# Kernel tuning notes

Measured on AMD Instinct MI355X. Metric: run time of the kernel, lower is better.

## Reference

```python
import jax, jax.numpy as jnp
import numpy as np

N, E = 50000, 800000
IN_DIM, HID, L, H = 128, 128, 3, 4
C = HID // H  # per-head channels
NEG_SLOPE = 0.2


def layer_norm(x, g, b, eps=1e-5):
    mu = jnp.mean(x, axis=-1, keepdims=True)
    var = jnp.var(x, axis=-1, keepdims=True)
    return (x - mu) * jax.lax.rsqrt(var + eps) * g + b


def gatv2_conv(x, edge_index, Wl, bl, Wr, br, att, conv_b):
    # x: [N, HID]; edge_index: [2, E]; Wl/Wr: [HID, HID]; att: [H, C]
    src, dst = edge_index[0], edge_index[1]
    xl = (x @ Wl + bl).reshape(N, H, C)  # source transform
    xr = (x @ Wr + br).reshape(N, H, C)  # target transform
    e = jax.nn.leaky_relu(xl[src] + xr[dst], NEG_SLOPE)      # [E, H, C]
    alpha = jnp.einsum('ehc,hc->eh', e, att)                  # [E, H]
    # segment softmax over incoming edges of each dst node
    amax = jax.ops.segment_max(alpha, dst, num_segments=N)    # [N, H]
    ex = jnp.exp(alpha - amax[dst])
    denom = jax.ops.segment_sum(ex, dst, num_segments=N)[dst] + 1e-16
    w = ex / denom                                            # [E, H]
    out = jax.ops.segment_sum(xl[src] * w[:, :, None], dst, num_segments=N)
    return out.reshape(N, HID) + conv_b


def setup_inputs() -> dict:
    key = jax.random.key(0)
    ks = jax.random.split(key, 24)
    s = 0.05
    inp = {
        'x': jax.random.normal(ks[0], (N, IN_DIM), jnp.float32),
        'edge_index': jax.random.randint(ks[1], (2, E), 0, N, jnp.int64),
        'Win': jax.random.normal(ks[2], (IN_DIM, HID)) * s,
        'b_in': jnp.zeros((HID,)),
        'ln_g': jnp.ones((L, HID)),
        'ln_b': jnp.zeros((L, HID)),
        'Wl': jax.random.normal(ks[3], (L, HID, HID)) * s,
        'bl': jnp.zeros((L, HID)),
        'Wr': jax.random.normal(ks[4], (L, HID, HID)) * s,
        'br': jnp.zeros((L, HID)),
        'att': jax.random.normal(ks[5], (L, H, C)) * s,
        'conv_b': jnp.zeros((L, HID)),
        'fn_g': jnp.ones((HID,)),
        'fn_b': jnp.zeros((HID,)),
        'pW1': jax.random.normal(ks[6], (HID, HID // 2)) * s,
        'pb1': jnp.zeros((HID // 2,)),
        'pW2': jax.random.normal(ks[7], (HID // 2, 1)) * s,
        'pb2': jnp.zeros((1,)),
        'vW1': jax.random.normal(ks[8], (HID, HID // 2)) * s,
        'vb1': jnp.zeros((HID // 2,)),
        'vW2': jax.random.normal(ks[9], (HID // 2, HID)) * s,
        'vb2': jnp.zeros((HID,)),
    }
    return inp


def reference(x, edge_index, Win, b_in, ln_g, ln_b, Wl, bl, Wr, br, att, conv_b,
              fn_g, fn_b, pW1, pb1, pW2, pb2, vW1, vb1, vW2, vb2):
    h = x @ Win + b_in  # input_proj
    # GNNResidualBlock (assumed pre-norm residual): h = h + gelu(conv(LN(h)))
    for i in range(L):
        z = layer_norm(h, ln_g[i], ln_b[i])
        z = gatv2_conv(z, edge_index, Wl[i], bl[i], Wr[i], br[i], att[i], conv_b[i])
        h = h + jax.nn.gelu(z)
    h = layer_norm(h, fn_g, fn_b)
    prob_logits = jax.nn.gelu(h @ pW1 + pb1) @ pW2 + pb2   # [N, 1]
    volume_emb = jax.nn.gelu(h @ vW1 + vb1) @ vW2 + vb2     # [N, HID]
    return (volume_emb, prob_logits)
```

## Files before the change

kernel.cpp:

```cpp
#include <hip/hip_runtime.h>
#include <math.h>

constexpr int NN  = 50000;
constexpr int EE  = 800000;

typedef short bf16x8 __attribute__((ext_vector_type(8)));
typedef float f32x4  __attribute__((ext_vector_type(4)));

__device__ __forceinline__ unsigned f2bfu(float f) {
    union { float f; unsigned u; } x; x.f = f;
    unsigned r = x.u + 0x7fffu + ((x.u >> 16) & 1u);
    return r >> 16;
}
__device__ __forceinline__ short f2bf(float f) { return (short)f2bfu(f); }
__device__ __forceinline__ unsigned pack2(float lo, float hi) {
    return f2bfu(lo) | (f2bfu(hi) << 16);
}
__device__ __forceinline__ float bfbits_lo(unsigned w) { return __uint_as_float(w << 16); }
__device__ __forceinline__ float bfbits_hi(unsigned w) { return __uint_as_float(w & 0xffff0000u); }

__device__ __forceinline__ float gelu_tanh(float x) {
    float u = 0.7978845608028654f * (x + 0.044715f * x * x * x);
    float t = 1.0f - 2.0f / (__expf(2.0f * u) + 1.0f);
    return 0.5f * x * (1.0f + t);
}

__device__ __forceinline__ float dpp_add16(float x) {
    int t;
    t = __builtin_amdgcn_update_dpp(0, __float_as_int(x), 0xB1,  0xf, 0xf, true);
    x += __int_as_float(t);
    t = __builtin_amdgcn_update_dpp(0, __float_as_int(x), 0x4E,  0xf, 0xf, true);
    x += __int_as_float(t);
    t = __builtin_amdgcn_update_dpp(0, __float_as_int(x), 0x141, 0xf, 0xf, true);
    x += __int_as_float(t);
    t = __builtin_amdgcn_update_dpp(0, __float_as_int(x), 0x140, 0xf, 0xf, true);
    x += __int_as_float(t);
    return x;
}

struct WtArgs {
    const float* src[10];
    short*       dst[10];
    int K[10];
    int N[10];
};

__global__ __launch_bounds__(256) void prep_weights(WtArgs a) {
    int m = blockIdx.x >> 4;
    int slice = blockIdx.x & 15;
    const float* s = a.src[m];
    short* d = a.dst[m];
    int K = a.K[m], N = a.N[m], total = K * N;
    for (int i = slice * 256 + threadIdx.x; i < total; i += 16 * 256) {
        int k = i / N, n = i - k * N;
        d[n * K + k] = f2bf(s[i]);
    }
}

template<int BN, int NB, int DO_LN, int ACT, int OUTBF0, int OUTBF1>
__global__ __launch_bounds__(256) void fused_ln_gemm(
    const float* __restrict__ A,
    const float* __restrict__ lg, const float* __restrict__ lb,
    const short* __restrict__ B0t, const float* __restrict__ bias0, void* __restrict__ C0,
    const short* __restrict__ B1t, const float* __restrict__ bias1, void* __restrict__ C1,
    int nrows)
{
    constexpr int K = 128, KP = 136, BM = 64;
    constexpr int NF = BN / 16;
    constexpr int CH = K / 8;
    __shared__ short As[BM * KP];
    __shared__ short Bs[BN * KP];

    const int tid  = threadIdx.x;
    const int row0 = blockIdx.x * BM;

    {
        int r = tid >> 2, q = tid & 3;
        int grow = row0 + r;
        bool ok = grow < nrows;
        float4 v[8];
        const float* src = A + (size_t)grow * K + q * 32;
#pragma unroll
        for (int i = 0; i < 8; ++i)
            v[i] = ok ? *reinterpret_cast<const float4*>(src + i * 4)
                      : make_float4(0.f, 0.f, 0.f, 0.f);
        if (DO_LN) {
            float s = 0.f, s2 = 0.f;
#pragma unroll
            for (int i = 0; i < 8; ++i) {
                s  += v[i].x + v[i].y + v[i].z + v[i].w;
                s2 += v[i].x * v[i].x + v[i].y * v[i].y + v[i].z * v[i].z + v[i].w * v[i].w;
            }
            s += __shfl_xor(s, 1); s2 += __shfl_xor(s2, 1);
            s += __shfl_xor(s, 2); s2 += __shfl_xor(s2, 2);
            float mean = s * (1.f / 128.f);
            float var  = s2 * (1.f / 128.f) - mean * mean;
            float rstd = rsqrtf(var + 1e-5f);
#pragma unroll
            for (int i = 0; i < 8; ++i) {
                float4 gg = *reinterpret_cast<const float4*>(lg + q * 32 + i * 4);
                float4 bb = *reinterpret_cast<const float4*>(lb + q * 32 + i * 4);
                v[i].x = (v[i].x - mean) * rstd * gg.x + bb.x;
                v[i].y = (v[i].y - mean) * rstd * gg.y + bb.y;
                v[i].z = (v[i].z - mean) * rstd * gg.z + bb.z;
                v[i].w = (v[i].w - mean) * rstd * gg.w + bb.w;
            }
        }
        short* dst = &As[r * KP + q * 32];
#pragma unroll
        for (int i = 0; i < 4; ++i) {
            uint4 w = make_uint4(pack2(v[2*i].x,   v[2*i].y),
                                 pack2(v[2*i].z,   v[2*i].w),
                                 pack2(v[2*i+1].x, v[2*i+1].y),
                                 pack2(v[2*i+1].z, v[2*i+1].w));
            *reinterpret_cast<uint4*>(dst + i * 8) = w;
        }
    }

    auto stageB = [&](const short* __restrict__ Bt) {
#pragma unroll
        for (int it = 0; it < BN * CH / 256; ++it) {
            int idx = tid + it * 256;
            int nn = idx / CH, j = idx % CH;
            *reinterpret_cast<uint4*>(&Bs[nn * KP + j * 8]) =
                *reinterpret_cast<const uint4*>(&Bt[nn * K + j * 8]);
        }
    };
    stageB(B0t);
    __syncthreads();

    const int wave = tid >> 6;
    const int lane = tid & 63;
    const int kg   = lane >> 4;
    const int lr   = lane & 15;

    bf16x8 afrag[4];
#pragma unroll
    for (int kk = 0; kk < 4; ++kk)
        afrag[kk] = *reinterpret_cast<const bf16x8*>(
            &As[(wave * 16 + lr) * KP + kk * 32 + kg * 8]);

    auto do_gemm = [&](const float* __restrict__ bias, void* __restrict__ Cv, bool outbf) {
        f32x4 acc[NF];
#pragma unroll
        for (int nf = 0; nf < NF; ++nf) acc[nf] = (f32x4){0.f, 0.f, 0.f, 0.f};
#pragma unroll
        for (int nf = 0; nf < NF; ++nf) {
#pragma unroll
            for (int kk = 0; kk < 4; ++kk) {
                bf16x8 bfrag = *reinterpret_cast<const bf16x8*>(
                    &Bs[(nf * 16 + lr) * KP + kk * 32 + kg * 8]);
                acc[nf] = __builtin_amdgcn_mfma_f32_16x16x32_bf16(
                    afrag[kk], bfrag, acc[nf], 0, 0, 0);
            }
        }
#pragma unroll
        for (int nf = 0; nf < NF; ++nf) {
            int col = nf * 16 + lr;
            float bi = bias[col];
#pragma unroll
            for (int j = 0; j < 4; ++j) {
                int row = row0 + wave * 16 + kg * 4 + j;
                if (row < nrows) {
                    float v = acc[nf][j] + bi;
                    if (ACT == 1) v = gelu_tanh(v);
                    if (outbf) ((short*)Cv)[(size_t)row * BN + col] = f2bf(v);
                    else       ((float*)Cv)[(size_t)row * BN + col] = v;
                }
            }
        }
    };

    do_gemm(bias0, C0, OUTBF0 != 0);
    if (NB == 2) {
        __syncthreads();
        stageB(B1t);
        __syncthreads();
        do_gemm(bias1, C1, OUTBF1 != 0);
    }
}

__global__ __launch_bounds__(256) void final_head_kernel(
    const float* __restrict__ A,
    const float* __restrict__ lg, const float* __restrict__ lb,
    const short* __restrict__ pW1t, const float* __restrict__ pb1,
    const float* __restrict__ pW2, const float* __restrict__ pb2,
    const short* __restrict__ vW1t, const float* __restrict__ vb1,
    short* __restrict__ t2, float* __restrict__ prob, int nrows)
{
    constexpr int K = 128, KP = 136, BM = 64;
    constexpr int CH = K / 8;
    __shared__ short As[BM * KP];
    __shared__ short Bs[128 * KP];

    const int tid  = threadIdx.x;
    const int row0 = blockIdx.x * BM;

    {
        int r = tid >> 2, q = tid & 3;
        int grow = row0 + r;
        bool ok = grow < nrows;
        float4 v[8];
        const float* src = A + (size_t)grow * K + q * 32;
#pragma unroll
        for (int i = 0; i < 8; ++i)
            v[i] = ok ? *reinterpret_cast<const float4*>(src + i * 4)
                      : make_float4(0.f, 0.f, 0.f, 0.f);
        float s = 0.f, s2 = 0.f;
#pragma unroll
        for (int i = 0; i < 8; ++i) {
            s  += v[i].x + v[i].y + v[i].z + v[i].w;
            s2 += v[i].x * v[i].x + v[i].y * v[i].y + v[i].z * v[i].z + v[i].w * v[i].w;
        }
        s += __shfl_xor(s, 1); s2 += __shfl_xor(s2, 1);
        s += __shfl_xor(s, 2); s2 += __shfl_xor(s2, 2);
        float mean = s * (1.f / 128.f);
        float var  = s2 * (1.f / 128.f) - mean * mean;
        float rstd = rsqrtf(var + 1e-5f);
        short* dst = &As[r * KP + q * 32];
#pragma unroll
        for (int i = 0; i < 8; ++i) {
            float4 gg = *reinterpret_cast<const float4*>(lg + q * 32 + i * 4);
            float4 bb = *reinterpret_cast<const float4*>(lb + q * 32 + i * 4);
            v[i].x = (v[i].x - mean) * rstd * gg.x + bb.x;
            v[i].y = (v[i].y - mean) * rstd * gg.y + bb.y;
            v[i].z = (v[i].z - mean) * rstd * gg.z + bb.z;
            v[i].w = (v[i].w - mean) * rstd * gg.w + bb.w;
        }
#pragma unroll
        for (int i = 0; i < 4; ++i) {
            uint4 w = make_uint4(pack2(v[2*i].x,   v[2*i].y),
                                 pack2(v[2*i].z,   v[2*i].w),
                                 pack2(v[2*i+1].x, v[2*i+1].y),
                                 pack2(v[2*i+1].z, v[2*i+1].w));
            *reinterpret_cast<uint4*>(dst + i * 8) = w;
        }
    }
#pragma unroll
    for (int it = 0; it < 8; ++it) {
        int idx = tid + it * 256;
        int nn = idx / CH, j = idx % CH;
        const short* srcw = (nn < 64) ? &pW1t[nn * K + j * 8]
                                      : &vW1t[(nn - 64) * K + j * 8];
        *reinterpret_cast<uint4*>(&Bs[nn * KP + j * 8]) =
            *reinterpret_cast<const uint4*>(srcw);
    }
    __syncthreads();

    const int wave = tid >> 6;
    const int lane = tid & 63;
    const int kg   = lane >> 4;
    const int lr   = lane & 15;

    bf16x8 afrag[4];
#pragma unroll
    for (int kk = 0; kk < 4; ++kk)
        afrag[kk] = *reinterpret_cast<const bf16x8*>(
            &As[(wave * 16 + lr) * KP + kk * 32 + kg * 8]);

    {
        f32x4 acc[4];
#pragma unroll
        for (int nf = 0; nf < 4; ++nf) acc[nf] = (f32x4){0.f, 0.f, 0.f, 0.f};
#pragma unroll
        for (int nf = 0; nf < 4; ++nf)
#pragma unroll
            for (int kk = 0; kk < 4; ++kk) {
                bf16x8 bfrag = *reinterpret_cast<const bf16x8*>(
                    &Bs[(64 + nf * 16 + lr) * KP + kk * 32 + kg * 8]);
                acc[nf] = __builtin_amdgcn_mfma_f32_16x16x32_bf16(
                    afrag[kk], bfrag, acc[nf], 0, 0, 0);
            }
#pragma unroll
        for (int nf = 0; nf < 4; ++nf) {
            int col = nf * 16 + lr;
            float bi = vb1[col];
#pragma unroll
            for (int j = 0; j < 4; ++j) {
                int row = row0 + wave * 16 + kg * 4 + j;
                if (row < nrows)
                    t2[(size_t)row * 64 + col] = f2bf(gelu_tanh(acc[nf][j] + bi));
            }
        }
    }
    {
        f32x4 acc[4];
#pragma unroll
        for (int nf = 0; nf < 4; ++nf) acc[nf] = (f32x4){0.f, 0.f, 0.f, 0.f};
#pragma unroll
        for (int nf = 0; nf < 4; ++nf)
#pragma unroll
            for (int kk = 0; kk < 4; ++kk) {
                bf16x8 bfrag = *reinterpret_cast<const bf16x8*>(
                    &Bs[(nf * 16 + lr) * KP + kk * 32 + kg * 8]);
                acc[nf] = __builtin_amdgcn_mfma_f32_16x16x32_bf16(
                    afrag[kk], bfrag, acc[nf], 0, 0, 0);
            }
        float pr[4] = {0.f, 0.f, 0.f, 0.f};
#pragma unroll
        for (int nf = 0; nf < 4; ++nf) {
            int col = nf * 16 + lr;
            float bi = pb1[col];
            float w2 = pW2[col];
#pragma unroll
            for (int j = 0; j < 4; ++j)
                pr[j] = fmaf(gelu_tanh(acc[nf][j] + bi), w2, pr[j]);
        }
#pragma unroll
        for (int j = 0; j < 4; ++j) {
            float v = dpp_add16(pr[j]);
            int row = row0 + wave * 16 + kg * 4 + j;
            if (lr == 0 && row < nrows) prob[row] = v + pb2[0];
        }
    }
}

template<int K, int BN, int ACT, int OUTBF>
__global__ __launch_bounds__(256) void gemm_mfma(
    const short* __restrict__ A, const short* __restrict__ Wt,
    const float* __restrict__ bias, void* __restrict__ Cv, int nrows)
{
    constexpr int BM = 64;
    constexpr int KP = K + 8;
    constexpr int NF = BN / 16;
    constexpr int KK = K / 32;
    constexpr int CH = K / 8;
    __shared__ short As[BM * KP];
    __shared__ short Bs[BN * KP];

    const int tid  = threadIdx.x;
    const int row0 = blockIdx.x * BM;

#pragma unroll
    for (int it = 0; it < BM * CH / 256; ++it) {
        int idx = tid + it * 256;
        int r = idx / CH, j = idx % CH;
        uint4 v = make_uint4(0u, 0u, 0u, 0u);
        if (row0 + r < nrows)
            v = *reinterpret_cast<const uint4*>(&A[(size_t)(row0 + r) * K + j * 8]);
        *reinterpret_cast<uint4*>(&As[r * KP + j * 8]) = v;
    }
#pragma unroll
    for (int it = 0; it < BN * CH / 256; ++it) {
        int idx = tid + it * 256;
        int n = idx / CH, j = idx % CH;
        *reinterpret_cast<uint4*>(&Bs[n * KP + j * 8]) =
            *reinterpret_cast<const uint4*>(&Wt[n * K + j * 8]);
    }
    __syncthreads();

    const int wave = tid >> 6;
    const int lane = tid & 63;
    const int kg   = lane >> 4;
    const int lr   = lane & 15;

    f32x4 acc[NF];
#pragma unroll
    for (int nf = 0; nf < NF; ++nf) acc[nf] = (f32x4){0.f, 0.f, 0.f, 0.f};

    bf16x8 afrag[KK];
#pragma unroll
    for (int kk = 0; kk < KK; ++kk)
        afrag[kk] = *reinterpret_cast<const bf16x8*>(
            &As[(wave * 16 + lr) * KP + kk * 32 + kg * 8]);

#pragma unroll
    for (int nf = 0; nf < NF; ++nf) {
#pragma unroll
        for (int kk = 0; kk < KK; ++kk) {
            bf16x8 bfrag = *reinterpret_cast<const bf16x8*>(
                &Bs[(nf * 16 + lr) * KP + kk * 32 + kg * 8]);
            acc[nf] = __builtin_amdgcn_mfma_f32_16x16x32_bf16(
                afrag[kk], bfrag, acc[nf], 0, 0, 0);
        }
    }

#pragma unroll
    for (int nf = 0; nf < NF; ++nf) {
        int col = nf * 16 + lr;
        float bi = bias[col];
#pragma unroll
        for (int j = 0; j < 4; ++j) {
            int row = row0 + wave * 16 + kg * 4 + j;
            if (row < nrows) {
                float v = acc[nf][j] + bi;
                if (ACT == 1) v = gelu_tanh(v);
                if (OUTBF) ((short*)Cv)[(size_t)row * BN + col] = f2bf(v);
                else       ((float*)Cv)[(size_t)row * BN + col] = v;
            }
        }
    }
}

__global__ void pos_kernel(const int* __restrict__ ei, int* __restrict__ counts,
                           int* __restrict__ pos) {
    int e = blockIdx.x * 256 + threadIdx.x;
    if (e < EE) pos[e] = atomicAdd(&counts[ei[EE + e]], 1);
}

__global__ __launch_bounds__(1024) void scan_kernel(const int* __restrict__ counts,
                                                    int* __restrict__ roff) {
    __shared__ int wsum[16];
    __shared__ int tilesum;
    int tid = threadIdx.x, wid = tid >> 6, lane = tid & 63;
    if (tid == 0) roff[0] = 0;
    int carry = 0;
    for (int base = 0; base < NN; base += 1024) {
        int idx = base + tid;
        int x = (idx < NN) ? counts[idx] : 0;
#pragma unroll
        for (int off = 1; off < 64; off <<= 1) {
            int t = __shfl_up(x, off);
            if (lane >= off) x += t;
        }
        if (lane == 63) wsum[wid] = x;
        __syncthreads();
        if (wid == 0) {
            int s = (lane < 16) ? wsum[lane] : 0;
#pragma unroll
            for (int off = 1; off < 16; off <<= 1) {
                int t = __shfl_up(s, off);
                if (lane >= off) s += t;
            }
            if (lane < 16) wsum[lane] = s;
            if (lane == 15) tilesum = s;
        }
        __syncthreads();
        int excl = (wid > 0) ? wsum[wid - 1] : 0;
        if (idx < NN) roff[idx + 1] = carry + excl + x;
        carry += tilesum;
        __syncthreads();
    }
}

__global__ void scatter_kernel(const int* __restrict__ ei, const int* __restrict__ roff,
                               const int* __restrict__ pos, int* __restrict__ ssrc) {
    int e = blockIdx.x * 256 + threadIdx.x;
    if (e < EE) {
        int d = ei[EE + e];
        ssrc[roff[d] + pos[e]] = ei[e] << 8;
    }
}

__global__ __launch_bounds__(256) void gat_node_kernel(
    const short* __restrict__ XL, const short* __restrict__ XR,
    const int* __restrict__ roff, const int* __restrict__ ssrc,
    const float* __restrict__ att, const float* __restrict__ conv_b,
    float* __restrict__ h)
{
    int n = blockIdx.x * 4 + (threadIdx.x >> 6);
    if (n >= NN) return;
    int lane = threadIdx.x & 63;
    int j0 = lane * 2;
    unsigned wr = *reinterpret_cast<const unsigned*>(&XR[(size_t)n * 128 + j0]);
    float xr0 = bfbits_lo(wr), xr1 = bfbits_hi(wr);
    float2 at = *reinterpret_cast<const float2*>(&att[j0]);

    float dA = 0.f, a0A = 0.f, a1A = 0.f;
    float dB = 0.f, a0B = 0.f, a1B = 0.f;

    const char* XLb = (const char*)XL;
    const unsigned lbyte = (unsigned)lane * 4u;

    auto proc = [&](unsigned w, float& d, float& a0, float& a1) {
        float x0 = bfbits_lo(w), x1 = bfbits_hi(w);
        float e0 = x0 + xr0; e0 = fmaxf(e0, 0.2f * e0);
        float e1 = x1 + xr1; e1 = fmaxf(e1, 0.2f * e1);
        float part = fmaf(e1, at.y, e0 * at.x);
        part = dpp_add16(part);
        float pe = __expf(part);
        d += pe;
        a0 = fmaf(pe, x0, a0);
        a1 = fmaf(pe, x1, a1);
    };

    int beg = roff[n], end = roff[n + 1], p = beg;
    for (; p + 3 < end; p += 4) {
        unsigned o0 = (unsigned)ssrc[p]     + lbyte;
        unsigned o1 = (unsigned)ssrc[p + 1] + lbyte;
        unsigned o2 = (unsigned)ssrc[p + 2] + lbyte;
        unsigned o3 = (unsigned)ssrc[p + 3] + lbyte;
        unsigned w0 = *reinterpret_cast<const unsigned*>(XLb + o0);
        unsigned w1 = *reinterpret_cast<const unsigned*>(XLb + o1);
        unsigned w2 = *reinterpret_cast<const unsigned*>(XLb + o2);
        unsigned w3 = *reinterpret_cast<const unsigned*>(XLb + o3);
        proc(w0, dA, a0A, a1A);
        proc(w1, dB, a0B, a1B);
        proc(w2, dA, a0A, a1A);
        proc(w3, dB, a0B, a1B);
    }
    for (; p < end; ++p) {
        unsigned w0 = *reinterpret_cast<const unsigned*>(
            XLb + ((unsigned)ssrc[p] + lbyte));
        proc(w0, dA, a0A, a1A);
    }
    float d    = dA + dB;
    float acc0 = a0A + a0B;
    float acc1 = a1A + a1B;

    float inv = 1.f / (d + 1e-16f);
    float2 cb = *reinterpret_cast<const float2*>(&conv_b[j0]);
    float o0 = gelu_tanh(fmaf(acc0, inv, cb.x));
    float o1 = gelu_tanh(fmaf(acc1, inv, cb.y));
    float2 hv = *reinterpret_cast<const float2*>(&h[(size_t)n * 128 + j0]);
    hv.x += o0; hv.y += o1;
    *reinterpret_cast<float2*>(&h[(size_t)n * 128 + j0]) = hv;
}

extern "C" void kernel_launch(void* const* d_in, const int* in_sizes, int n_in,
                              void* d_out, int out_size, void* d_ws, size_t ws_size,
                              hipStream_t stream)
{
    const float* x      = (const float*)d_in[0];
    const int*   ei     = (const int*)  d_in[1];
    const float* Win    = (const float*)d_in[2];
    const float* b_in   = (const float*)d_in[3];
    const float* ln_g   = (const float*)d_in[4];
    const float* ln_b   = (const float*)d_in[5];
    const float* Wl     = (const float*)d_in[6];
    const float* bl     = (const float*)d_in[7];
    const float* Wr     = (const float*)d_in[8];
    const float* br     = (const float*)d_in[9];
    const float* att    = (const float*)d_in[10];
    const float* conv_b = (const float*)d_in[11];
    const float* fn_g   = (const float*)d_in[12];
    const float* fn_b   = (const float*)d_in[13];
    const float* pW1    = (const float*)d_in[14];
    const float* pb1    = (const float*)d_in[15];
    const float* pW2    = (const float*)d_in[16];
    const float* pb2    = (const float*)d_in[17];
    const float* vW1    = (const float*)d_in[18];
    const float* vb1    = (const float*)d_in[19];
    const float* vW2    = (const float*)d_in[20];
    const float* vb2    = (const float*)d_in[21];

    char* wp = (char*)d_ws;
    float* h   = (float*)wp;  wp += (size_t)NN * 128 * 4;
    short* XL  = (short*)wp;  wp += (size_t)NN * 128 * 2;
    short* XR  = (short*)wp;  wp += (size_t)NN * 128 * 2;
    int* counts = (int*)wp;   wp += (size_t)NN * 4;
    int* roff   = (int*)wp;   wp += (size_t)(NN + 16) * 4;
    int* pos    = (int*)wp;   wp += (size_t)EE * 4;
    int* ssrc   = (int*)wp;   wp += (size_t)EE * 4;
    short* Win_t = (short*)wp;
    short* Wl_t  = Win_t + 16384;
    short* Wr_t  = Wl_t + 3 * 16384;
    short* pW1_t = Wr_t + 3 * 16384;
    short* vW1_t = pW1_t + 8192;
    short* vW2_t = vW1_t + 8192;
    short* t2 = XL;
    float* vol  = (float*)d_out;
    float* prob = (float*)d_out + (size_t)NN * 128;

    WtArgs wa;
    wa.src[0] = Win;  wa.dst[0] = Win_t; wa.K[0] = 128; wa.N[0] = 128;
    for (int i = 0; i < 3; ++i) {
        wa.src[1 + i] = Wl + (size_t)i * 16384; wa.dst[1 + i] = Wl_t + i * 16384;
        wa.K[1 + i] = 128; wa.N[1 + i] = 128;
        wa.src[4 + i] = Wr + (size_t)i * 16384; wa.dst[4 + i] = Wr_t + i * 16384;
        wa.K[4 + i] = 128; wa.N[4 + i] = 128;
    }
    wa.src[7] = pW1; wa.dst[7] = pW1_t; wa.K[7] = 128; wa.N[7] = 64;
    wa.src[8] = vW1; wa.dst[8] = vW1_t; wa.K[8] = 128; wa.N[8] = 64;
    wa.src[9] = vW2; wa.dst[9] = vW2_t; wa.K[9] = 64;  wa.N[9] = 128;
    prep_weights<<<160, 256, 0, stream>>>(wa);

    hipMemsetAsync(counts, 0, (size_t)NN * sizeof(int), stream);
    pos_kernel<<<(EE + 255) / 256, 256, 0, stream>>>(ei, counts, pos);
    scan_kernel<<<1, 1024, 0, stream>>>(counts, roff);
    scatter_kernel<<<(EE + 255) / 256, 256, 0, stream>>>(ei, roff, pos, ssrc);

    const int gemm_grid = (NN + 63) / 64;
    const int row_grid  = (NN + 3) / 4;

    fused_ln_gemm<128, 1, 0, 0, 0, 0><<<gemm_grid, 256, 0, stream>>>(
        x, nullptr, nullptr, Win_t, b_in, h, nullptr, nullptr, nullptr, NN);

    for (int i = 0; i < 3; ++i) {
        fused_ln_gemm<128, 2, 1, 0, 1, 1><<<gemm_grid, 256, 0, stream>>>(
            h, ln_g + i * 128, ln_b + i * 128,
            Wl_t + i * 16384, bl + i * 128, XL,
            Wr_t + i * 16384, br + i * 128, XR, NN);
        gat_node_kernel<<<row_grid, 256, 0, stream>>>(
            XL, XR, roff, ssrc, att + i * 128, conv_b + i * 128, h);
    }

    final_head_kernel<<<gemm_grid, 256, 0, stream>>>(
        h, fn_g, fn_b, pW1_t, pb1, pW2, pb2, vW1_t, vb1, t2, prob, NN);

    gemm_mfma<64, 128, 0, 0><<<gemm_grid, 256, 0, stream>>>(t2, vW2_t, vb2, vol, NN);
}
```

Baseline: 414.9 us.

## Process four edges per wavefront with 16-byte row loads in GAT aggregation

Restructures the per-node GATv2 aggregation so each wavefront splits into four 16-lane groups. Each group handles a different incoming edge, and each lane loads 8 bf16 channels with a single 16-byte load instead of 2 channels per lane. The 32-channel head reduction becomes a 4-lane DPP reduction, and partial sums are combined across groups with shuffles before only 16 lanes write the output. This is meant to cut per-edge instruction and reduction overhead and use wider memory transactions, at the cost of idle lanes on tail iterations and extra cross-group shuffles.

```diff
diff --git a/kernel.cpp b/kernel.cpp
--- a/kernel.cpp
+++ b/kernel.cpp
@@ -34,6 +34,15 @@
     t = __builtin_amdgcn_update_dpp(0, __float_as_int(x), 0x141, 0xf, 0xf, true);
     x += __int_as_float(t);
     t = __builtin_amdgcn_update_dpp(0, __float_as_int(x), 0x140, 0xf, 0xf, true);
+    x += __int_as_float(t);
+    return x;
+}
+
+__device__ __forceinline__ float dpp_add4(float x) {
+    int t;
+    t = __builtin_amdgcn_update_dpp(0, __float_as_int(x), 0xB1, 0xf, 0xf, true);
+    x += __int_as_float(t);
+    t = __builtin_amdgcn_update_dpp(0, __float_as_int(x), 0x4E, 0xf, 0xf, true);
     x += __int_as_float(t);
     return x;
 }
@@ -450,61 +459,85 @@
 {
     int n = blockIdx.x * 4 + (threadIdx.x >> 6);
     if (n >= NN) return;
-    int lane = threadIdx.x & 63;
-    int j0 = lane * 2;
-    unsigned wr = *reinterpret_cast<const unsigned*>(&XR[(size_t)n * 128 + j0]);
-    float xr0 = bfbits_lo(wr), xr1 = bfbits_hi(wr);
-    float2 at = *reinterpret_cast<const float2*>(&att[j0]);
-
-    float dA = 0.f, a0A = 0.f, a1A = 0.f;
-    float dB = 0.f, a0B = 0.f, a1B = 0.f;
+    const int lane = threadIdx.x & 63;
+    const int slot = lane >> 4;
+    const int pos  = lane & 15;
+    const unsigned cboff = (unsigned)pos * 16u;
+
+    float xr[8];
+    {
+        uint4 w4 = *reinterpret_cast<const uint4*>(&XR[(size_t)n * 128 + pos * 8]);
+        xr[0] = bfbits_lo(w4.x); xr[1] = bfbits_hi(w4.x);
+        xr[2] = bfbits_lo(w4.y); xr[3] = bfbits_hi(w4.y);
+        xr[4] = bfbits_lo(w4.z); xr[5] = bfbits_hi(w4.z);
+        xr[6] = bfbits_lo(w4.w); xr[7] = bfbits_hi(w4.w);
+    }
+    float at[8];
+    {
+        float4 a0 = *reinterpret_cast<const float4*>(&att[pos * 8]);
+        float4 a1 = *reinterpret_cast<const float4*>(&att[pos * 8 + 4]);
+        at[0] = a0.x; at[1] = a0.y; at[2] = a0.z; at[3] = a0.w;
+        at[4] = a1.x; at[5] = a1.y; at[6] = a1.z; at[7] = a1.w;
+    }
+
+    float d = 0.f;
+    float acc[8];
+#pragma unroll
+    for (int c = 0; c < 8; ++c) acc[c] = 0.f;
 
     const char* XLb = (const char*)XL;
-    const unsigned lbyte = (unsigned)lane * 4u;
-
-    auto proc = [&](unsigned w, float& d, float& a0, float& a1) {
-        float x0 = bfbits_lo(w), x1 = bfbits_hi(w);
-        float e0 = x0 + xr0; e0 = fmaxf(e0, 0.2f * e0);
-        float e1 = x1 + xr1; e1 = fmaxf(e1, 0.2f * e1);
-        float part = fmaf(e1, at.y, e0 * at.x);
-        part = dpp_add16(part);
-        float pe = __expf(part);
+    const int beg = roff[n], end = roff[n + 1];
+
+    for (int p0 = beg; p0 < end; p0 += 4) {
+        int p = p0 + slot;
+        bool valid = p < end;
+        int pc = valid ? p : beg;
+        unsigned off = (unsigned)ssrc[pc] + cboff;
+        uint4 w4 = *reinterpret_cast<const uint4*>(XLb + off);
+        float xl[8];
+        xl[0] = bfbits_lo(w4.x); xl[1] = bfbits_hi(w4.x);
+        xl[2] = bfbits_lo(w4.y); xl[3] = bfbits_hi(w4.y);
+        xl[4] = bfbits_lo(w4.z); xl[5] = bfbits_hi(w4.z);
+        xl[6] = bfbits_lo(w4.w); xl[7] = bfbits_hi(w4.w);
+        float part = 0.f;
+#pragma unroll
+        for (int c = 0; c < 8; ++c) {
+            float e = xl[c] + xr[c];
+            e = fmaxf(e, 0.2f * e);
+            part = fmaf(e, at[c], part);
+        }
+        part = dpp_add4(part);
+        float pe = valid ? __expf(part) : 0.f;
         d += pe;
-        a0 = fmaf(pe, x0, a0);
-        a1 = fmaf(pe, x1, a1);
-    };
-
-    int beg = roff[n], end = roff[n + 1], p = beg;
-    for (; p + 3 < end; p += 4) {
-        unsigned o0 = (unsigned)ssrc[p]     + lbyte;
-        unsigned o1 = (unsigned)ssrc[p + 1] + lbyte;
-        unsigned o2 = (unsigned)ssrc[p + 2] + lbyte;
-        unsigned o3 = (unsigned)ssrc[p + 3] + lbyte;
-        unsigned w0 = *reinterpret_cast<const unsigned*>(XLb + o0);
-        unsigned w1 = *reinterpret_cast<const unsigned*>(XLb + o1);
-        unsigned w2 = *reinterpret_cast<const unsigned*>(XLb + o2);
-        unsigned w3 = *reinterpret_cast<const unsigned*>(XLb + o3);
-        proc(w0, dA, a0A, a1A);
-        proc(w1, dB, a0B, a1B);
-        proc(w2, dA, a0A, a1A);
-        proc(w3, dB, a0B, a1B);
-    }
-    for (; p < end; ++p) {
-        unsigned w0 = *reinterpret_cast<const unsigned*>(
-            XLb + ((unsigned)ssrc[p] + lbyte));
-        proc(w0, dA, a0A, a1A);
-    }
-    float d    = dA + dB;
-    float acc0 = a0A + a0B;
-    float acc1 = a1A + a1B;
-
-    float inv = 1.f / (d + 1e-16f);
-    float2 cb = *reinterpret_cast<const float2*>(&conv_b[j0]);
-    float o0 = gelu_tanh(fmaf(acc0, inv, cb.x));
-    float o1 = gelu_tanh(fmaf(acc1, inv, cb.y));
-    float2 hv = *reinterpret_cast<const float2*>(&h[(size_t)n * 128 + j0]);
-    hv.x += o0; hv.y += o1;
-    *reinterpret_cast<float2*>(&h[(size_t)n * 128 + j0]) = hv;
+#pragma unroll
+        for (int c = 0; c < 8; ++c) acc[c] = fmaf(pe, xl[c], acc[c]);
+    }
+
+    d += __shfl_xor(d, 16); d += __shfl_xor(d, 32);
+#pragma unroll
+    for (int c = 0; c < 8; ++c) {
+        acc[c] += __shfl_xor(acc[c], 16);
+        acc[c] += __shfl_xor(acc[c], 32);
+    }
+
+    if (lane < 16) {
+        float inv = 1.f / (d + 1e-16f);
+        float* hp = &h[(size_t)n * 128 + pos * 8];
+        float4 h0 = *reinterpret_cast<const float4*>(hp);
+        float4 h1 = *reinterpret_cast<const float4*>(hp + 4);
+        float4 c0 = *reinterpret_cast<const float4*>(&conv_b[pos * 8]);
+        float4 c1 = *reinterpret_cast<const float4*>(&conv_b[pos * 8 + 4]);
+        h0.x += gelu_tanh(fmaf(acc[0], inv, c0.x));
+        h0.y += gelu_tanh(fmaf(acc[1], inv, c0.y));
+        h0.z += gelu_tanh(fmaf(acc[2], inv, c0.z));
+        h0.w += gelu_tanh(fmaf(acc[3], inv, c0.w));
+        h1.x += gelu_tanh(fmaf(acc[4], inv, c1.x));
+        h1.y += gelu_tanh(fmaf(acc[5], inv, c1.y));
+        h1.z += gelu_tanh(fmaf(acc[6], inv, c1.z));
+        h1.w += gelu_tanh(fmaf(acc[7], inv, c1.w));
+        *reinterpret_cast<float4*>(hp)     = h0;
+        *reinterpret_cast<float4*>(hp + 4) = h1;
+    }
 }
 
 extern "C" void kernel_launch(void* const* d_in, const int* in_sizes, int n_in,
```

Measured after the change: 425.7 us. 1.03x slower.

## Merge independent preprocessing and GEMM stages into hybrid kernels and fuse final head

Applied to the files above, without the earlier changes.

Combines independent stages into shared launches: the edge-count pass runs alongside weight prep, the prefix scan alongside the input projection GEMM, and the CSR scatter alongside the first layer's LN+GEMM. The scan is widened to process four counts per thread over a padded node count. The final head now performs the second volume GEMM in the same kernel, keeping the GELU intermediate in shared memory instead of writing it to global memory. The aim is fewer launches, more overlap of small serial stages, and less global traffic. The trade-off is that one-block scan work now shares a grid with GEMM blocks, and the larger hybrid kernels may lose occupancy.

```diff
diff --git a/kernel.cpp b/kernel.cpp
--- a/kernel.cpp
+++ b/kernel.cpp
@@ -3,6 +3,7 @@
 
 constexpr int NN  = 50000;
 constexpr int EE  = 800000;
+constexpr int NPAD = 50176;
 
 typedef short bf16x8 __attribute__((ext_vector_type(8)));
 typedef float f32x4  __attribute__((ext_vector_type(4)));
@@ -45,34 +46,18 @@
     int N[10];
 };
 
-__global__ __launch_bounds__(256) void prep_weights(WtArgs a) {
-    int m = blockIdx.x >> 4;
-    int slice = blockIdx.x & 15;
-    const float* s = a.src[m];
-    short* d = a.dst[m];
-    int K = a.K[m], N = a.N[m], total = K * N;
-    for (int i = slice * 256 + threadIdx.x; i < total; i += 16 * 256) {
-        int k = i / N, n = i - k * N;
-        d[n * K + k] = f2bf(s[i]);
-    }
-}
-
 template<int BN, int NB, int DO_LN, int ACT, int OUTBF0, int OUTBF1>
-__global__ __launch_bounds__(256) void fused_ln_gemm(
-    const float* __restrict__ A,
+__device__ __forceinline__ void ln_gemm_body(
+    int row0, const float* __restrict__ A,
     const float* __restrict__ lg, const float* __restrict__ lb,
     const short* __restrict__ B0t, const float* __restrict__ bias0, void* __restrict__ C0,
     const short* __restrict__ B1t, const float* __restrict__ bias1, void* __restrict__ C1,
-    int nrows)
-{
-    constexpr int K = 128, KP = 136, BM = 64;
+    int nrows, short* As, short* Bs)
+{
+    constexpr int K = 128, KP = 136;
     constexpr int NF = BN / 16;
     constexpr int CH = K / 8;
-    __shared__ short As[BM * KP];
-    __shared__ short Bs[BN * KP];
-
-    const int tid  = threadIdx.x;
-    const int row0 = blockIdx.x * BM;
+    const int tid = threadIdx.x;
 
     {
         int r = tid >> 2, q = tid & 3;
@@ -180,234 +165,35 @@
     }
 }
 
-__global__ __launch_bounds__(256) void final_head_kernel(
-    const float* __restrict__ A,
-    const float* __restrict__ lg, const float* __restrict__ lb,
-    const short* __restrict__ pW1t, const float* __restrict__ pb1,
-    const float* __restrict__ pW2, const float* __restrict__ pb2,
-    const short* __restrict__ vW1t, const float* __restrict__ vb1,
-    short* __restrict__ t2, float* __restrict__ prob, int nrows)
-{
-    constexpr int K = 128, KP = 136, BM = 64;
-    constexpr int CH = K / 8;
-    __shared__ short As[BM * KP];
-    __shared__ short Bs[128 * KP];
-
-    const int tid  = threadIdx.x;
-    const int row0 = blockIdx.x * BM;
-
-    {
-        int r = tid >> 2, q = tid & 3;
-        int grow = row0 + r;
-        bool ok = grow < nrows;
-        float4 v[8];
-        const float* src = A + (size_t)grow * K + q * 32;
-#pragma unroll
-        for (int i = 0; i < 8; ++i)
-            v[i] = ok ? *reinterpret_cast<const float4*>(src + i * 4)
-                      : make_float4(0.f, 0.f, 0.f, 0.f);
-        float s = 0.f, s2 = 0.f;
-#pragma unroll
-        for (int i = 0; i < 8; ++i) {
-            s  += v[i].x + v[i].y + v[i].z + v[i].w;
-            s2 += v[i].x * v[i].x + v[i].y * v[i].y + v[i].z * v[i].z + v[i].w * v[i].w;
-        }
-        s += __shfl_xor(s, 1); s2 += __shfl_xor(s2, 1);
-        s += __shfl_xor(s, 2); s2 += __shfl_xor(s2, 2);
-        float mean = s * (1.f / 128.f);
-        float var  = s2 * (1.f / 128.f) - mean * mean;
-        float rstd = rsqrtf(var + 1e-5f);
-        short* dst = &As[r * KP + q * 32];
-#pragma unroll
-        for (int i = 0; i < 8; ++i) {
-            float4 gg = *reinterpret_cast<const float4*>(lg + q * 32 + i * 4);
-            float4 bb = *reinterpret_cast<const float4*>(lb + q * 32 + i * 4);
-            v[i].x = (v[i].x - mean) * rstd * gg.x + bb.x;
-            v[i].y = (v[i].y - mean) * rstd * gg.y + bb.y;
-            v[i].z = (v[i].z - mean) * rstd * gg.z + bb.z;
-            v[i].w = (v[i].w - mean) * rstd * gg.w + bb.w;
-        }
-#pragma unroll
-        for (int i = 0; i < 4; ++i) {
-            uint4 w = make_uint4(pack2(v[2*i].x,   v[2*i].y),
-                                 pack2(v[2*i].z,   v[2*i].w),
-                                 pack2(v[2*i+1].x, v[2*i+1].y),
-                                 pack2(v[2*i+1].z, v[2*i+1].w));
-            *reinterpret_cast<uint4*>(dst + i * 8) = w;
-        }
-    }
-#pragma unroll
-    for (int it = 0; it < 8; ++it) {
-        int idx = tid + it * 256;
-        int nn = idx / CH, j = idx % CH;
-        const short* srcw = (nn < 64) ? &pW1t[nn * K + j * 8]
-                                      : &vW1t[(nn - 64) * K + j * 8];
-        *reinterpret_cast<uint4*>(&Bs[nn * KP + j * 8]) =
-            *reinterpret_cast<const uint4*>(srcw);
-    }
-    __syncthreads();
-
-    const int wave = tid >> 6;
-    const int lane = tid & 63;
-    const int kg   = lane >> 4;
-    const int lr   = lane & 15;
-
-    bf16x8 afrag[4];
-#pragma unroll
-    for (int kk = 0; kk < 4; ++kk)
-        afrag[kk] = *reinterpret_cast<const bf16x8*>(
-            &As[(wave * 16 + lr) * KP + kk * 32 + kg * 8]);
-
-    {
-        f32x4 acc[4];
-#pragma unroll
-        for (int nf = 0; nf < 4; ++nf) acc[nf] = (f32x4){0.f, 0.f, 0.f, 0.f};
-#pragma unroll
-        for (int nf = 0; nf < 4; ++nf)
-#pragma unroll
-            for (int kk = 0; kk < 4; ++kk) {
-                bf16x8 bfrag = *reinterpret_cast<const bf16x8*>(
-                    &Bs[(64 + nf * 16 + lr) * KP + kk * 32 + kg * 8]);
-                acc[nf] = __builtin_amdgcn_mfma_f32_16x16x32_bf16(
-                    afrag[kk], bfrag, acc[nf], 0, 0, 0);
-            }
-#pragma unroll
-        for (int nf = 0; nf < 4; ++nf) {
-            int col = nf * 16 + lr;
-            float bi = vb1[col];
-#pragma unroll
-            for (int j = 0; j < 4; ++j) {
-                int row = row0 + wave * 16 + kg * 4 + j;
-                if (row < nrows)
-                    t2[(size_t)row * 64 + col] = f2bf(gelu_tanh(acc[nf][j] + bi));
-            }
-        }
-    }
-    {
-        f32x4 acc[4];
-#pragma unroll
-        for (int nf = 0; nf < 4; ++nf) acc[nf] = (f32x4){0.f, 0.f, 0.f, 0.f};
-#pragma unroll
-        for (int nf = 0; nf < 4; ++nf)
-#pragma unroll
-            for (int kk = 0; kk < 4; ++kk) {
-                bf16x8 bfrag = *reinterpret_cast<const bf16x8*>(
-                    &Bs[(nf * 16 + lr) * KP + kk * 32 + kg * 8]);
-                acc[nf] = __builtin_amdgcn_mfma_f32_16x16x32_bf16(
-                    afrag[kk], bfrag, acc[nf], 0, 0, 0);
-            }
-        float pr[4] = {0.f, 0.f, 0.f, 0.f};
-#pragma unroll
-        for (int nf = 0; nf < 4; ++nf) {
-            int col = nf * 16 + lr;
-            float bi = pb1[col];
-            float w2 = pW2[col];
-#pragma unroll
-            for (int j = 0; j < 4; ++j)
-                pr[j] = fmaf(gelu_tanh(acc[nf][j] + bi), w2, pr[j]);
-        }
-#pragma unroll
-        for (int j = 0; j < 4; ++j) {
-            float v = dpp_add16(pr[j]);
-            int row = row0 + wave * 16 + kg * 4 + j;
-            if (lr == 0 && row < nrows) prob[row] = v + pb2[0];
-        }
-    }
-}
-
-template<int K, int BN, int ACT, int OUTBF>
-__global__ __launch_bounds__(256) void gemm_mfma(
-    const short* __restrict__ A, const short* __restrict__ Wt,
-    const float* __restrict__ bias, void* __restrict__ Cv, int nrows)
-{
-    constexpr int BM = 64;
-    constexpr int KP = K + 8;
-    constexpr int NF = BN / 16;
-    constexpr int KK = K / 32;
-    constexpr int CH = K / 8;
-    __shared__ short As[BM * KP];
-    __shared__ short Bs[BN * KP];
-
-    const int tid  = threadIdx.x;
-    const int row0 = blockIdx.x * BM;
-
-#pragma unroll
-    for (int it = 0; it < BM * CH / 256; ++it) {
-        int idx = tid + it * 256;
-        int r = idx / CH, j = idx % CH;
-        uint4 v = make_uint4(0u, 0u, 0u, 0u);
-        if (row0 + r < nrows)
-            v = *reinterpret_cast<const uint4*>(&A[(size_t)(row0 + r) * K + j * 8]);
-        *reinterpret_cast<uint4*>(&As[r * KP + j * 8]) = v;
-    }
-#pragma unroll
-    for (int it = 0; it < BN * CH / 256; ++it) {
-        int idx = tid + it * 256;
-        int n = idx / CH, j = idx % CH;
-        *reinterpret_cast<uint4*>(&Bs[n * KP + j * 8]) =
-            *reinterpret_cast<const uint4*>(&Wt[n * K + j * 8]);
-    }
-    __syncthreads();
-
-    const int wave = tid >> 6;
-    const int lane = tid & 63;
-    const int kg   = lane >> 4;
-    const int lr   = lane & 15;
-
-    f32x4 acc[NF];
-#pragma unroll
-    for (int nf = 0; nf < NF; ++nf) acc[nf] = (f32x4){0.f, 0.f, 0.f, 0.f};
-
-    bf16x8 afrag[KK];
-#pragma unroll
-    for (int kk = 0; kk < KK; ++kk)
-        afrag[kk] = *reinterpret_cast<const bf16x8*>(
-            &As[(wave * 16 + lr) * KP + kk * 32 + kg * 8]);
-
-#pragma unroll
-    for (int nf = 0; nf < NF; ++nf) {
-#pragma unroll
-        for (int kk = 0; kk < KK; ++kk) {
-            bf16x8 bfrag = *reinterpret_cast<const bf16x8*>(
-                &Bs[(nf * 16 + lr) * KP + kk * 32 + kg * 8]);
-            acc[nf] = __builtin_amdgcn_mfma_f32_16x16x32_bf16(
-                afrag[kk], bfrag, acc[nf], 0, 0, 0);
-        }
-    }
-
-#pragma unroll
-    for (int nf = 0; nf < NF; ++nf) {
-        int col = nf * 16 + lr;
-        float bi = bias[col];
-#pragma unroll
-        for (int j = 0; j < 4; ++j) {
-            int row = row0 + wave * 16 + kg * 4 + j;
-            if (row < nrows) {
-                float v = acc[nf][j] + bi;
-                if (ACT == 1) v = gelu_tanh(v);
-                if (OUTBF) ((short*)Cv)[(size_t)row * BN + col] = f2bf(v);
-                else       ((float*)Cv)[(size_t)row * BN + col] = v;
-            }
-        }
-    }
-}
-
-__global__ void pos_kernel(const int* __restrict__ ei, int* __restrict__ counts,
-                           int* __restrict__ pos) {
-    int e = blockIdx.x * 256 + threadIdx.x;
-    if (e < EE) pos[e] = atomicAdd(&counts[ei[EE + e]], 1);
-}
-
-__global__ __launch_bounds__(1024) void scan_kernel(const int* __restrict__ counts,
-                                                    int* __restrict__ roff) {
-    __shared__ int wsum[16];
+__global__ __launch_bounds__(256) void hybrid1(
+    const int* __restrict__ ei, int* __restrict__ counts, int* __restrict__ pos, WtArgs a)
+{
+    if (blockIdx.x < 1024) {
+        for (int e = blockIdx.x * 256 + threadIdx.x; e < EE; e += 1024 * 256)
+            pos[e] = atomicAdd(&counts[ei[EE + e]], 1);
+    } else {
+        int bb = blockIdx.x - 1024;
+        int m = bb >> 4, slice = bb & 15;
+        const float* s = a.src[m];
+        short* d = a.dst[m];
+        int K = a.K[m], N = a.N[m], total = K * N;
+        for (int i = slice * 256 + threadIdx.x; i < total; i += 16 * 256) {
+            int k = i / N, n = i - k * N;
+            d[n * K + k] = f2bf(s[i]);
+        }
+    }
+}
+
+__device__ void scan256(const int* __restrict__ counts, int* __restrict__ roff) {
+    __shared__ int wsum[4];
     __shared__ int tilesum;
     int tid = threadIdx.x, wid = tid >> 6, lane = tid & 63;
-    if (tid == 0) roff[0] = 0;
     int carry = 0;
-    for (int base = 0; base < NN; base += 1024) {
-        int idx = base + tid;
-        int x = (idx < NN) ? counts[idx] : 0;
+    for (int base = 0; base < NPAD; base += 1024) {
+        int idx = base + tid * 4;
+        int4 c = *reinterpret_cast<const int4*>(&counts[idx]);
+        int s0 = c.x, s1 = s0 + c.y, s2 = s1 + c.z, s3 = s2 + c.w;
+        int x = s3;
 #pragma unroll
         for (int off = 1; off < 64; off <<= 1) {
             int t = __shfl_up(x, off);
@@ -415,31 +201,64 @@
         }
         if (lane == 63) wsum[wid] = x;
         __syncthreads();
-        if (wid == 0) {
-            int s = (lane < 16) ? wsum[lane] : 0;
-#pragma unroll
-            for (int off = 1; off < 16; off <<= 1) {
-                int t = __shfl_up(s, off);
-                if (lane >= off) s += t;
-            }
-            if (lane < 16) wsum[lane] = s;
-            if (lane == 15) tilesum = s;
+        if (tid == 0) {
+            int a0 = wsum[0], a1 = wsum[1], a2 = wsum[2], a3 = wsum[3];
+            wsum[0] = 0; wsum[1] = a0; wsum[2] = a0 + a1; wsum[3] = a0 + a1 + a2;
+            tilesum = a0 + a1 + a2 + a3;
         }
         __syncthreads();
-        int excl = (wid > 0) ? wsum[wid - 1] : 0;
-        if (idx < NN) roff[idx + 1] = carry + excl + x;
+        int start = carry + wsum[wid] + (x - s3);
+        int4 o = make_int4(start, start + s0, start + s1, start + s2);
+        *reinterpret_cast<int4*>(&roff[idx]) = o;
         carry += tilesum;
         __syncthreads();
     }
 }
 
-__global__ void scatter_kernel(const int* __restrict__ ei, const int* __restrict__ roff,
-                               const int* __restrict__ pos, int* __restrict__ ssrc) {
-    int e = blockIdx.x * 256 + threadIdx.x;
-    if (e < EE) {
-        int d = ei[EE + e];
-        ssrc[roff[d] + pos[e]] = ei[e] << 8;
-    }
+__global__ __launch_bounds__(256) void hybrid2(
+    const int* __restrict__ counts, int* __restrict__ roff,
+    const float* __restrict__ x, const short* __restrict__ Win_t,
+    const float* __restrict__ b_in, float* __restrict__ h, int nrows)
+{
+    __shared__ short As[64 * 136];
+    __shared__ short Bs[128 * 136];
+    if (blockIdx.x == 0) {
+        scan256(counts, roff);
+    } else {
+        ln_gemm_body<128, 1, 0, 0, 0, 0>((blockIdx.x - 1) * 64, x, nullptr, nullptr,
+            Win_t, b_in, h, nullptr, nullptr, nullptr, nrows, As, Bs);
+    }
+}
+
+__global__ __launch_bounds__(256) void hybrid3(
+    const int* __restrict__ ei, const int* __restrict__ roff,
+    const int* __restrict__ pos, int* __restrict__ ssrc,
+    const float* __restrict__ h, const float* __restrict__ lg, const float* __restrict__ lb,
+    const short* __restrict__ Wl_t, const float* __restrict__ bl, short* __restrict__ XL,
+    const short* __restrict__ Wr_t, const float* __restrict__ br, short* __restrict__ XR,
+    int nrows)
+{
+    __shared__ short As[64 * 136];
+    __shared__ short Bs[128 * 136];
+    if (blockIdx.x < 512) {
+        for (int e = blockIdx.x * 256 + threadIdx.x; e < EE; e += 512 * 256)
+            ssrc[roff[ei[EE + e]] + pos[e]] = ei[e] << 8;
+    } else {
+        ln_gemm_body<128, 2, 1, 0, 1, 1>((blockIdx.x - 512) * 64, h, lg, lb,
+            Wl_t, bl, XL, Wr_t, br, XR, nrows, As, Bs);
+    }
+}
+
+__global__ __launch_bounds__(256) void fused_layer(
+    const float* __restrict__ h, const float* __restrict__ lg, const float* __restrict__ lb,
+    const short* __restrict__ Wl_t, const float* __restrict__ bl, short* __restrict__ XL,
+    const short* __restrict__ Wr_t, const float* __restrict__ br, short* __restrict__ XR,
+    int nrows)
+{
+    __shared__ short As[64 * 136];
+    __shared__ short Bs[128 * 136];
+    ln_gemm_body<128, 2, 1, 0, 1, 1>(blockIdx.x * 64, h, lg, lb,
+        Wl_t, bl, XL, Wr_t, br, XR, nrows, As, Bs);
 }
 
 __global__ __launch_bounds__(256) void gat_node_kernel(
@@ -505,6 +324,180 @@
     float2 hv = *reinterpret_cast<const float2*>(&h[(size_t)n * 128 + j0]);
     hv.x += o0; hv.y += o1;
     *reinterpret_cast<float2*>(&h[(size_t)n * 128 + j0]) = hv;
+}
+
+__global__ __launch_bounds__(256) void final_head_full(
+    const float* __restrict__ A,
+    const float* __restrict__ lg, const float* __restrict__ lb,
+    const short* __restrict__ pW1t, const float* __restrict__ pb1,
+    const float* __restrict__ pW2, const float* __restrict__ pb2,
+    const short* __restrict__ vW1t, const float* __restrict__ vb1,
+    const short* __restrict__ vW2t, const float* __restrict__ vb2,
+    float* __restrict__ vol, float* __restrict__ prob, int nrows)
+{
+    constexpr int K = 128, KP = 136, KP2 = 72;
+    constexpr int CH = K / 8;
+    __shared__ short As[64 * 136];
+    __shared__ short Bs[128 * 136];
+
+    const int tid  = threadIdx.x;
+    const int row0 = blockIdx.x * 64;
+
+    {
+        int r = tid >> 2, q = tid & 3;
+        int grow = row0 + r;
+        bool ok = grow < nrows;
+        float4 v[8];
+        const float* src = A + (size_t)grow * K + q * 32;
+#pragma unroll
+        for (int i = 0; i < 8; ++i)
+            v[i] = ok ? *reinterpret_cast<const float4*>(src + i * 4)
+                      : make_float4(0.f, 0.f, 0.f, 0.f);
+        float s = 0.f, s2 = 0.f;
+#pragma unroll
+        for (int i = 0; i < 8; ++i) {
+            s  += v[i].x + v[i].y + v[i].z + v[i].w;
+            s2 += v[i].x * v[i].x + v[i].y * v[i].y + v[i].z * v[i].z + v[i].w * v[i].w;
+        }
+        s += __shfl_xor(s, 1); s2 += __shfl_xor(s2, 1);
+        s += __shfl_xor(s, 2); s2 += __shfl_xor(s2, 2);
+        float mean = s * (1.f / 128.f);
+        float var  = s2 * (1.f / 128.f) - mean * mean;
+        float rstd = rsqrtf(var + 1e-5f);
+        short* dst = &As[r * KP + q * 32];
+#pragma unroll
+        for (int i = 0; i < 8; ++i) {
+            float4 gg = *reinterpret_cast<const float4*>(lg + q * 32 + i * 4);
+            float4 bb = *reinterpret_cast<const float4*>(lb + q * 32 + i * 4);
+            v[i].x = (v[i].x - mean) * rstd * gg.x + bb.x;
+            v[i].y = (v[i].y - mean) * rstd * gg.y + bb.y;
+            v[i].z = (v[i].z - mean) * rstd * gg.z + bb.z;
+            v[i].w = (v[i].w - mean) * rstd * gg.w + bb.w;
+        }
+#pragma unroll
+        for (int i = 0; i < 4; ++i) {
+            uint4 w = make_uint4(pack2(v[2*i].x,   v[2*i].y),
+                                 pack2(v[2*i].z,   v[2*i].w),
+                                 pack2(v[2*i+1].x, v[2*i+1].y),
+                                 pack2(v[2*i+1].z, v[2*i+1].w));
+            *reinterpret_cast<uint4*>(dst + i * 8) = w;
+        }
+    }
+#pragma unroll
+    for (int it = 0; it < 8; ++it) {
+        int idx = tid + it * 256;
+        int nn = idx / CH, j = idx % CH;
+        const short* srcw = (nn < 64) ? &pW1t[nn * K + j * 8]
+                                      : &vW1t[(nn - 64) * K + j * 8];
+        *reinterpret_cast<uint4*>(&Bs[nn * KP + j * 8]) =
+            *reinterpret_cast<const uint4*>(srcw);
+    }
+    __syncthreads();
+
+    const int wave = tid >> 6;
+    const int lane = tid & 63;
+    const int kg   = lane >> 4;
+    const int lr   = lane & 15;
+
+    bf16x8 afrag[4];
+#pragma unroll
+    for (int kk = 0; kk < 4; ++kk)
+        afrag[kk] = *reinterpret_cast<const bf16x8*>(
+            &As[(wave * 16 + lr) * KP + kk * 32 + kg * 8]);
+
+    f32x4 acc_v[4];
+#pragma unroll
+    for (int nf = 0; nf < 4; ++nf) acc_v[nf] = (f32x4){0.f, 0.f, 0.f, 0.f};
+#pragma unroll
+    for (int nf = 0; nf < 4; ++nf)
+#pragma unroll
+        for (int kk = 0; kk < 4; ++kk) {
+            bf16x8 bfrag = *reinterpret_cast<const bf16x8*>(
+                &Bs[(64 + nf * 16 + lr) * KP + kk * 32 + kg * 8]);
+            acc_v[nf] = __builtin_amdgcn_mfma_f32_16x16x32_bf16(
+                afrag[kk], bfrag, acc_v[nf], 0, 0, 0);
+        }
+
+    {
+        f32x4 acc[4];
+#pragma unroll
+        for (int nf = 0; nf < 4; ++nf) acc[nf] = (f32x4){0.f, 0.f, 0.f, 0.f};
+#pragma unroll
+        for (int nf = 0; nf < 4; ++nf)
+#pragma unroll
+            for (int kk = 0; kk < 4; ++kk) {
+                bf16x8 bfrag = *reinterpret_cast<const bf16x8*>(
+                    &Bs[(nf * 16 + lr) * KP + kk * 32 + kg * 8]);
+                acc[nf] = __builtin_amdgcn_mfma_f32_16x16x32_bf16(
+                    afrag[kk], bfrag, acc[nf], 0, 0, 0);
+            }
+        float pr[4] = {0.f, 0.f, 0.f, 0.f};
+#pragma unroll
+        for (int nf = 0; nf < 4; ++nf) {
+            int col = nf * 16 + lr;
+            float bi = pb1[col];
+            float w2 = pW2[col];
+#pragma unroll
+            for (int j = 0; j < 4; ++j)
+                pr[j] = fmaf(gelu_tanh(acc[nf][j] + bi), w2, pr[j]);
+        }
+#pragma unroll
+        for (int j = 0; j < 4; ++j) {
+            float v = dpp_add16(pr[j]);
+            int row = row0 + wave * 16 + kg * 4 + j;
+            if (lr == 0 && row < nrows) prob[row] = v + pb2[0];
+        }
+    }
+
+    __syncthreads();
+    short* t2lds = As;
+#pragma unroll
+    for (int nf = 0; nf < 4; ++nf) {
+        int col = nf * 16 + lr;
+        float bi = vb1[col];
+#pragma unroll
+        for (int j = 0; j < 4; ++j) {
+            int r = wave * 16 + kg * 4 + j;
+            t2lds[r * KP2 + col] = f2bf(gelu_tanh(acc_v[nf][j] + bi));
+        }
+    }
+#pragma unroll
+    for (int it = 0; it < 4; ++it) {
+        int idx = tid + it * 256;
+        int nn = idx >> 3, j = idx & 7;
+        *reinterpret_cast<uint4*>(&Bs[nn * KP2 + j * 8]) =
+            *reinterpret_cast<const uint4*>(&vW2t[nn * 64 + j * 8]);
+    }
+    __syncthreads();
+
+    bf16x8 a2[2];
+#pragma unroll
+    for (int kk = 0; kk < 2; ++kk)
+        a2[kk] = *reinterpret_cast<const bf16x8*>(
+            &t2lds[(wave * 16 + lr) * KP2 + kk * 32 + kg * 8]);
+    f32x4 accv[8];
+#pragma unroll
+    for (int nf = 0; nf < 8; ++nf) accv[nf] = (f32x4){0.f, 0.f, 0.f, 0.f};
+#pragma unroll
+    for (int nf = 0; nf < 8; ++nf)
+#pragma unroll
+        for (int kk = 0; kk < 2; ++kk) {
+            bf16x8 bfrag = *reinterpret_cast<const bf16x8*>(
+                &Bs[(nf * 16 + lr) * KP2 + kk * 32 + kg * 8]);
+            accv[nf] = __builtin_amdgcn_mfma_f32_16x16x32_bf16(
+                a2[kk], bfrag, accv[nf], 0, 0, 0);
+        }
+#pragma unroll
+    for (int nf = 0; nf < 8; ++nf) {
+        int col = nf * 16 + lr;
+        float bi = vb2[col];
+#pragma unroll
+        for (int j = 0; j < 4; ++j) {
+            int row = row0 + wave * 16 + kg * 4 + j;
+            if (row < nrows)
+                vol[(size_t)row * 128 + col] = accv[nf][j] + bi;
+        }
+    }
 }
 
 extern "C" void kernel_launch(void* const* d_in, const int* in_sizes, int n_in,
@@ -538,8 +531,8 @@
     float* h   = (float*)wp;  wp += (size_t)NN * 128 * 4;
     short* XL  = (short*)wp;  wp += (size_t)NN * 128 * 2;
     short* XR  = (short*)wp;  wp += (size_t)NN * 128 * 2;
-    int* counts = (int*)wp;   wp += (size_t)NN * 4;
-    int* roff   = (int*)wp;   wp += (size_t)(NN + 16) * 4;
+    int* counts = (int*)wp;   wp += (size_t)NPAD * 4;
+    int* roff   = (int*)wp;   wp += (size_t)(NPAD + 16) * 4;
     int* pos    = (int*)wp;   wp += (size_t)EE * 4;
     int* ssrc   = (int*)wp;   wp += (size_t)EE * 4;
     short* Win_t = (short*)wp;
@@ -548,7 +541,6 @@
     short* pW1_t = Wr_t + 3 * 16384;
     short* vW1_t = pW1_t + 8192;
     short* vW2_t = vW1_t + 8192;
-    short* t2 = XL;
     float* vol  = (float*)d_out;
     float* prob = (float*)d_out + (size_t)NN * 128;
 
@@ -563,30 +555,25 @@
     wa.src[7] = pW1; wa.dst[7] = pW1_t; wa.K[7] = 128; wa.N[7] = 64;
     wa.src[8] = vW1; wa.dst[8] = vW1_t; wa.K[8] = 128; wa.N[8] = 64;
     wa.src[9] = vW2; wa.dst[9] = vW2_t; wa.K[9] = 64;  wa.N[9] = 128;
-    prep_weights<<<160, 256, 0, stream>>>(wa);
-
-    hipMemsetAsync(counts, 0, (size_t)NN * sizeof(int), stream);
-    pos_kernel<<<(EE + 255) / 256, 256, 0, stream>>>(ei, counts, pos);
-    scan_kernel<<<1, 1024, 0, stream>>>(counts, roff);
-    scatter_kernel<<<(EE + 255) / 256, 256, 0, stream>>>(ei, roff, pos, ssrc);
 
     const int gemm_grid = (NN + 63) / 64;
     const int row_grid  = (NN + 3) / 4;
 
-    fused_ln_gemm<128, 1, 0, 0, 0, 0><<<gemm_grid, 256, 0, stream>>>(
-        x, nullptr, nullptr, Win_t, b_in, h, nullptr, nullptr, nullptr, NN);
-
-    for (int i = 0; i < 3; ++i) {
-        fused_ln_gemm<128, 2, 1, 0, 1, 1><<<gemm_grid, 256, 0, stream>>>(
+    hipMemsetAsync(counts, 0, (size_t)NPAD * sizeof(int), stream);
+    hybrid1<<<1024 + 160, 256, 0, stream>>>(ei, counts, pos, wa);
+    hybrid2<<<1 + gemm_grid, 256, 0, stream>>>(counts, roff, x, Win_t, b_in, h, NN);
+    hybrid3<<<512 + gemm_grid, 256, 0, stream>>>(ei, roff, pos, ssrc,
+        h, ln_g, ln_b, Wl_t, bl, XL, Wr_t, br, XR, NN);
+    gat_node_kernel<<<row_grid, 256, 0, stream>>>(
+        XL, XR, roff, ssrc, att, conv_b, h);
+    for (int i = 1; i < 3; ++i) {
+        fused_layer<<<gemm_grid, 256, 0, stream>>>(
             h, ln_g + i * 128, ln_b + i * 128,
             Wl_t + i * 16384, bl + i * 128, XL,
             Wr_t + i * 16384, br + i * 128, XR, NN);
         gat_node_kernel<<<row_grid, 256, 0, stream>>>(
             XL, XR, roff, ssrc, att + i * 128, conv_b + i * 128, h);
     }
-
-    final_head_kernel<<<gemm_grid, 256, 0, stream>>>(
-        h, fn_g, fn_b, pW1_t, pb1, pW2, pb2, vW1_t, vb1, t2, prob, NN);
-
-    gemm_mfma<64, 128, 0, 0><<<gemm_grid, 256, 0, stream>>>(t2, vW2_t, vb2, vol, NN);
-}
+    final_head_full<<<gemm_grid, 256, 0, stream>>>(
+        h, fn_g, fn_b, pW1_t, pb1, pW2, pb2, vW1_t, vb1, vW2_t, vb2, vol, prob, NN);
+}
```

Measured after the change: 376.4 us. 9.3% less time.
